# Performance work log

Hardware: AMD Instinct MI355X
Metric: run time of the kernel (lower is better)

The kernel has to match this reference:

```python
import jax, jax.numpy as jnp
import numpy as np

D_MODEL = 1024
NUM_HEADS = 16
D_K = D_MODEL // NUM_HEADS
THETA = 10000.0


def setup_inputs() -> dict:
    key = jax.random.key(0)
    ks = jax.random.split(key, 5)
    b, s = 4, 1024
    std = 1.0 / np.sqrt(D_MODEL)
    x = jax.random.normal(ks[0], (b, s, D_MODEL), dtype=jnp.float32)
    token_positions = jnp.tile(jnp.arange(s, dtype=jnp.int64)[None, :], (b, 1))
    Wq = jax.random.truncated_normal(ks[1], -3.0, 3.0, (D_MODEL, D_MODEL), jnp.float32) * std
    Wk = jax.random.truncated_normal(ks[2], -3.0, 3.0, (D_MODEL, D_MODEL), jnp.float32) * std
    Wv = jax.random.truncated_normal(ks[3], -3.0, 3.0, (D_MODEL, D_MODEL), jnp.float32) * std
    Wo = jax.random.truncated_normal(ks[4], -3.0, 3.0, (D_MODEL, D_MODEL), jnp.float32) * std
    return {"x": x, "token_positions": token_positions,
            "Wq": Wq, "Wk": Wk, "Wv": Wv, "Wo": Wo}


def _apply_rope(x):
    # x: [b, h, s, d_k]; source uses row index i (ignores token_positions)
    s, d = x.shape[-2], x.shape[-1]
    pos = jnp.arange(s, dtype=jnp.float32)                      # [s]
    kidx = jnp.arange(0, d, 2, dtype=jnp.float32)               # [d/2]
    ang = pos[:, None] / (THETA ** (kidx / d))                  # [s, d/2]
    cos, sin = jnp.cos(ang), jnp.sin(ang)
    x_even, x_odd = x[..., 0::2], x[..., 1::2]                  # [b,h,s,d/2]
    out_even = x_even * cos - x_odd * sin
    out_odd = x_even * sin + x_odd * cos
    return jnp.stack([out_even, out_odd], axis=-1).reshape(x.shape)


def reference(x, token_positions, Wq, Wk, Wv, Wo):
    b, s, _ = x.shape
    # Linear: einsum '... din, dout din -> ... dout'  => x @ W.T
    q = jnp.einsum('bsd,ed->bse', x, Wq)
    k = jnp.einsum('bsd,ed->bse', x, Wk)
    v = jnp.einsum('bsd,ed->bse', x, Wv)
    # split heads -> [b, h, s, d_k]
    def split(t):
        return t.reshape(b, s, NUM_HEADS, D_K).transpose(0, 2, 1, 3)
    q, k, v = split(q), split(k), split(v)
    q = _apply_rope(q)
    k = _apply_rope(k)
    scores = jnp.einsum('bhqd,bhkd->bhqk', q, k) / np.sqrt(D_K)
    causal = jnp.tril(jnp.ones((s, s), dtype=bool))
    scores = jnp.where(causal, scores, -jnp.inf)
    attn = jax.nn.softmax(scores, axis=-1)
    out = jnp.einsum('bhqk,bhkd->bhqd', attn, v)
    out = out.transpose(0, 2, 1, 3).reshape(b, s, D_MODEL)
    return jnp.einsum('bsd,ed->bse', out, Wo)
```

## Files before the change

kernel.cpp:

```cpp
#include <hip/hip_runtime.h>

typedef __attribute__((ext_vector_type(8))) short short8;
typedef __attribute__((ext_vector_type(8))) __bf16 bf16x8;
typedef __attribute__((ext_vector_type(4))) float f32x4;
typedef __attribute__((ext_vector_type(4))) float float4v;
typedef __attribute__((ext_vector_type(4))) unsigned short ushort4v;
typedef __attribute__((ext_vector_type(2))) unsigned uint2v;

#define AS1 __attribute__((address_space(1)))
#define AS3 __attribute__((address_space(3)))

#define BATCH 4
#define SEQ 1024
#define DM 1024
#define NH 16
#define DKH 64
#define MROWS (BATCH * SEQ)
#define N3 (3 * DM)

static __device__ __forceinline__ unsigned short f2bf(float f) {
  unsigned u = __builtin_bit_cast(unsigned, f);
  u += 0x7FFFu + ((u >> 16) & 1u);
  return (unsigned short)(u >> 16);
}
static __device__ __forceinline__ float bf2f(unsigned short h) {
  return __builtin_bit_cast(float, ((unsigned)h) << 16);
}
static __device__ __forceinline__ unsigned cvt_pk_bf16(float lo, float hi) {
  unsigned r;
  asm("v_cvt_pk_bf16_f32 %0, %1, %2" : "=v"(r) : "v"(lo), "v"(hi));
  return r;
}
static __device__ __forceinline__ f32x4 mfma16(short8 a, short8 b, f32x4 c) {
  return __builtin_amdgcn_mfma_f32_16x16x32_bf16(
      __builtin_bit_cast(bf16x8, a), __builtin_bit_cast(bf16x8, b), c, 0, 0, 0);
}

__global__ __launch_bounds__(256) void convert_kernel(
    const float* __restrict__ x, const float* __restrict__ wq,
    const float* __restrict__ wk, const float* __restrict__ wv,
    const float* __restrict__ wo, unsigned short* __restrict__ xb,
    unsigned short* __restrict__ wqkv, unsigned short* __restrict__ wob) {
  size_t i4 = ((size_t)blockIdx.x * 256 + threadIdx.x) * 4;
  const size_t SZX = (size_t)MROWS * DM;
  const size_t SZW = (size_t)DM * DM;
  const float* src;
  unsigned short* dst;
  size_t off;
  if (i4 < SZX) {
    src = x; dst = xb; off = i4;
  } else if (i4 < SZX + SZW) {
    src = wq; dst = wqkv; off = i4 - SZX;
  } else if (i4 < SZX + 2 * SZW) {
    src = wk; dst = wqkv + SZW; off = i4 - SZX - SZW;
  } else if (i4 < SZX + 3 * SZW) {
    src = wv; dst = wqkv + 2 * SZW; off = i4 - SZX - 2 * SZW;
  } else {
    src = wo; dst = wob; off = i4 - SZX - 3 * SZW;
  }
  float4v v = *(const float4v*)(src + off);
  uint2v o;
  o.x = cvt_pk_bf16(v.x, v.y);
  o.y = cvt_pk_bf16(v.z, v.w);
  *(uint2v*)(dst + off) = o;
}

static __device__ __forceinline__ void store_c(float* p, float v) { *p = v; }
static __device__ __forceinline__ void store_c(unsigned short* p, float v) { *p = f2bf(v); }

template <typename OutT>
__global__ __launch_bounds__(256) void gemm_bt(
    const unsigned short* __restrict__ A, const unsigned short* __restrict__ B,
    OutT* __restrict__ C, int M, int N, int K) {
  __shared__ char sA[16384];
  __shared__ char sB[16384];
  const int tid = threadIdx.x, w = tid >> 6, lane = tid & 63;
  const int g = lane >> 4, r = lane & 15;
  const int m0 = blockIdx.y * 128, n0 = blockIdx.x * 128;
  const int wm = (w >> 1) * 64, wn = (w & 1) * 64;
  f32x4 acc[4][4] = {};
  for (int k0 = 0; k0 < K; k0 += 64) {
#pragma unroll
    for (int c = 0; c < 4; ++c) {
      int p = c * 4096 + tid * 16;
      int o = p ^ (((p >> 7) & 7) << 4);
      int row = o >> 7, colb = o & 127;
      const char* ga = (const char*)(A + (size_t)(m0 + row) * K + k0) + colb;
      const char* gb = (const char*)(B + (size_t)(n0 + row) * K + k0) + colb;
      __builtin_amdgcn_global_load_lds((const AS1 void*)ga,
                                       (AS3 void*)(sA + c * 4096 + (w << 10)), 16, 0, 0);
      __builtin_amdgcn_global_load_lds((const AS1 void*)gb,
                                       (AS3 void*)(sB + c * 4096 + (w << 10)), 16, 0, 0);
    }
    __syncthreads();
#pragma unroll
    for (int kk = 0; kk < 2; ++kk) {
      short8 af[4], bfr[4];
#pragma unroll
      for (int i = 0; i < 4; ++i) {
        int ra = wm + i * 16 + r;
        af[i] = *(const short8*)(sA + (((ra << 7) + (kk << 6) + (g << 4)) ^ ((ra & 7) << 4)));
        int rb = wn + i * 16 + r;
        bfr[i] = *(const short8*)(sB + (((rb << 7) + (kk << 6) + (g << 4)) ^ ((rb & 7) << 4)));
      }
#pragma unroll
      for (int i = 0; i < 4; ++i)
#pragma unroll
        for (int j = 0; j < 4; ++j) acc[i][j] = mfma16(af[i], bfr[j], acc[i][j]);
    }
    __syncthreads();
  }
#pragma unroll
  for (int i = 0; i < 4; ++i)
#pragma unroll
    for (int j = 0; j < 4; ++j)
#pragma unroll
      for (int jj = 0; jj < 4; ++jj) {
        int row = m0 + wm + i * 16 + g * 4 + jj;
        int col = n0 + wn + j * 16 + r;
        store_c(&C[(size_t)row * N + col], acc[i][j][jj]);
      }
}

__global__ __launch_bounds__(256) void rope_tv(const unsigned short* __restrict__ cf,
                                               unsigned short* __restrict__ qb,
                                               unsigned short* __restrict__ kb,
                                               unsigned short* __restrict__ vt) {
  __shared__ unsigned short tile[64][72];
  const int bid = blockIdx.x;
  if (bid < 8192) {
    int i = bid * 256 + threadIdx.x;
    int k = i & 31, h = (i >> 5) & 15, s = (i >> 9) & 1023, b = i >> 19;
    float freq = __expf(-(float)k * 0.28782313662425572f);
    float ang = (float)s * freq;
    float sn, cs;
    __sincosf(ang, &sn, &cs);
    const unsigned short* src = cf + (size_t)(b * SEQ + s) * N3 + h * DKH + 2 * k;
    float qe = bf2f(src[0]), qo = bf2f(src[1]);
    float ke = bf2f(src[DM]), ko = bf2f(src[DM + 1]);
    float q0 = (qe * cs - qo * sn) * 0.125f;
    float q1 = (qe * sn + qo * cs) * 0.125f;
    float k0 = ke * cs - ko * sn;
    float k1 = ke * sn + ko * cs;
    size_t dsto = (size_t)((b * NH + h) * SEQ + s) * DKH + 2 * k;
    *(unsigned*)(qb + dsto) = cvt_pk_bf16(q0, q1);
    *(unsigned*)(kb + dsto) = cvt_pk_bf16(k0, k1);
  } else {
    int t = bid - 8192;
    int bh = t >> 4, b = bh >> 4, h = bh & 15, s0 = (t & 15) * 64;
    int tt = threadIdx.x, row = tt >> 2, c0 = (tt & 3) * 16;
    const unsigned short* src = cf + (size_t)(b * SEQ + s0 + row) * N3 + 2 * DM + h * DKH + c0;
    short8 v0 = *(const short8*)src;
    short8 v1 = *(const short8*)(src + 8);
    *(short8*)&tile[row][c0] = v0;
    *(short8*)&tile[row][c0 + 8] = v1;
    __syncthreads();
    unsigned short* dst = vt + ((size_t)bh * DKH + row) * SEQ + s0 + c0;
    short8 o0, o1;
#pragma unroll
    for (int j = 0; j < 8; ++j) o0[j] = (short)tile[c0 + j][row];
#pragma unroll
    for (int j = 0; j < 8; ++j) o1[j] = (short)tile[c0 + 8 + j][row];
    *(short8*)dst = o0;
    *(short8*)(dst + 8) = o1;
  }
}

__global__ __launch_bounds__(256) void attn_kernel(const unsigned short* __restrict__ qb,
                                                   const unsigned short* __restrict__ kb,
                                                   const unsigned short* __restrict__ vt,
                                                   unsigned short* __restrict__ ob) {
  __shared__ char kl[2][8192];
  __shared__ char vl[2][8192];
  __shared__ unsigned short plds[4][2][1024];
  const int bx = blockIdx.x, bh = blockIdx.y, b = bh >> 4, h = bh & 15;
  const int qlo = bx, qhi = 15 - bx;
  const int tid = threadIdx.x, w = tid >> 6, lane = tid & 63;
  const int g = lane >> 4, r = lane & 15;
  const unsigned short* Q = qb + (size_t)bh * SEQ * DKH;
  const char* Kp = (const char*)(kb + (size_t)bh * SEQ * DKH);
  const char* Vp = (const char*)(vt + (size_t)bh * DKH * SEQ);

  const int p0 = (w << 10) + lane * 16;
  const int p1 = p0 + 4096;
  const int o0 = p0 ^ (((p0 >> 7) & 7) << 4);
  const int o1 = p1 ^ (((p1 >> 7) & 7) << 4);
  const int r0 = o0 >> 7, c0 = o0 & 127, r1 = o1 >> 7, c1 = o1 & 127;
  const size_t ks0 = (size_t)r0 * 128 + c0, ks1 = (size_t)r1 * 128 + c1;
  const size_t vs0 = (size_t)r0 * 2048 + c0, vs1 = (size_t)r1 * 2048 + c1;

#define STAGE_KV(bi, kt)                                                          \
  do {                                                                            \
    const char* kbase = Kp + (size_t)(kt) * 8192;                                 \
    const char* vbase = Vp + (size_t)(kt) * 128;                                  \
    __builtin_amdgcn_global_load_lds((const AS1 void*)(kbase + ks0),              \
                                     (AS3 void*)(kl[bi] + p0), 16, 0, 0);         \
    __builtin_amdgcn_global_load_lds((const AS1 void*)(kbase + ks1),              \
                                     (AS3 void*)(kl[bi] + p1), 16, 0, 0);         \
    __builtin_amdgcn_global_load_lds((const AS1 void*)(vbase + vs0),              \
                                     (AS3 void*)(vl[bi] + p0), 16, 0, 0);         \
    __builtin_amdgcn_global_load_lds((const AS1 void*)(vbase + vs1),              \
                                     (AS3 void*)(vl[bi] + p1), 16, 0, 0);         \
  } while (0)

  short8 qfL0, qfL1, qfH0, qfH1;
  {
    int qrL = qlo * 64 + w * 16 + r;
    int qrH = qhi * 64 + w * 16 + r;
    qfL0 = *(const short8*)(Q + (size_t)qrL * DKH + g * 8);
    qfL1 = *(const short8*)(Q + (size_t)qrL * DKH + 32 + g * 8);
    qfH0 = *(const short8*)(Q + (size_t)qrH * DKH + g * 8);
    qfH1 = *(const short8*)(Q + (size_t)qrH * DKH + 32 + g * 8);
  }
  f32x4 oaccL[4] = {}, oaccH[4] = {};
  float mrunL = -1e30f, lrunL = 0.f, mrunH = -1e30f, lrunH = 0.f;
  const int qgH = qhi * 64 + w * 16 + r;
  const int qgL = qlo * 64 + w * 16 + r;
  char* pbH = (char*)&plds[w][0][0];
  char* pbL = (char*)&plds[w][1][0];

  STAGE_KV(0, 0);
  __syncthreads();

  for (int kt = 0; kt <= qhi; ++kt) {
    if (kt < qhi) STAGE_KV((kt + 1) & 1, kt + 1);
    const bool doLo = (kt <= qlo);
    const char* kb_ = kl[kt & 1];
    const char* vb_ = vl[kt & 1];
    f32x4 sh[4] = {}, sl[4] = {};
#pragma unroll
    for (int nb = 0; nb < 4; ++nb) {
      int ra = nb * 16 + r;
      short8 kf0 = *(const short8*)(kb_ + ((ra * 128 + g * 16) ^ ((ra & 7) << 4)));
      short8 kf1 = *(const short8*)(kb_ + ((ra * 128 + 64 + g * 16) ^ ((ra & 7) << 4)));
      sh[nb] = mfma16(kf0, qfH0, sh[nb]);
      sh[nb] = mfma16(kf1, qfH1, sh[nb]);
      if (doLo) {
        sl[nb] = mfma16(kf0, qfL0, sl[nb]);
        sl[nb] = mfma16(kf1, qfL1, sl[nb]);
      }
    }
    if (kt == qhi) {
#pragma unroll
      for (int nb = 0; nb < 4; ++nb)
#pragma unroll
        for (int j = 0; j < 4; ++j)
          if (kt * 64 + nb * 16 + g * 4 + j > qgH) sh[nb][j] = -1e30f;
    }
    if (kt == qlo) {
#pragma unroll
      for (int nb = 0; nb < 4; ++nb)
#pragma unroll
        for (int j = 0; j < 4; ++j)
          if (kt * 64 + nb * 16 + g * 4 + j > qgL) sl[nb][j] = -1e30f;
    }
    float sclH, sclL = 1.f;
    {
      float a0 = fmaxf(fmaxf(sh[0][0], sh[0][1]), fmaxf(sh[0][2], sh[0][3]));
      float a1 = fmaxf(fmaxf(sh[1][0], sh[1][1]), fmaxf(sh[1][2], sh[1][3]));
      float a2 = fmaxf(fmaxf(sh[2][0], sh[2][1]), fmaxf(sh[2][2], sh[2][3]));
      float a3 = fmaxf(fmaxf(sh[3][0], sh[3][1]), fmaxf(sh[3][2], sh[3][3]));
      float tm = fmaxf(fmaxf(a0, a1), fmaxf(a2, a3));
      tm = fmaxf(tm, __shfl_xor(tm, 16, 64));
      tm = fmaxf(tm, __shfl_xor(tm, 32, 64));
      float mnew = fmaxf(mrunH, tm);
      sclH = __expf(mrunH - mnew);
      mrunH = mnew;
      float ps = 0.f;
#pragma unroll
      for (int nb = 0; nb < 4; ++nb)
#pragma unroll
        for (int j = 0; j < 4; ++j) {
          float p = __expf(sh[nb][j] - mnew);
          sh[nb][j] = p;
          ps += p;
        }
      ps += __shfl_xor(ps, 16, 64);
      ps += __shfl_xor(ps, 32, 64);
      lrunH = lrunH * sclH + ps;
#pragma unroll
      for (int nb = 0; nb < 4; ++nb) {
        uint2v pk;
        pk.x = cvt_pk_bf16(sh[nb][0], sh[nb][1]);
        pk.y = cvt_pk_bf16(sh[nb][2], sh[nb][3]);
        *(uint2v*)(pbH + ((r * 128 + nb * 32 + g * 8) ^ ((r & 7) << 4))) = pk;
      }
    }
    if (doLo) {
      float a0 = fmaxf(fmaxf(sl[0][0], sl[0][1]), fmaxf(sl[0][2], sl[0][3]));
      float a1 = fmaxf(fmaxf(sl[1][0], sl[1][1]), fmaxf(sl[1][2], sl[1][3]));
      float a2 = fmaxf(fmaxf(sl[2][0], sl[2][1]), fmaxf(sl[2][2], sl[2][3]));
      float a3 = fmaxf(fmaxf(sl[3][0], sl[3][1]), fmaxf(sl[3][2], sl[3][3]));
      float tm = fmaxf(fmaxf(a0, a1), fmaxf(a2, a3));
      tm = fmaxf(tm, __shfl_xor(tm, 16, 64));
      tm = fmaxf(tm, __shfl_xor(tm, 32, 64));
      float mnew = fmaxf(mrunL, tm);
      sclL = __expf(mrunL - mnew);
      mrunL = mnew;
      float ps = 0.f;
#pragma unroll
      for (int nb = 0; nb < 4; ++nb)
#pragma unroll
        for (int j = 0; j < 4; ++j) {
          float p = __expf(sl[nb][j] - mnew);
          sl[nb][j] = p;
          ps += p;
        }
      ps += __shfl_xor(ps, 16, 64);
      ps += __shfl_xor(ps, 32, 64);
      lrunL = lrunL * sclL + ps;
#pragma unroll
      for (int nb = 0; nb < 4; ++nb) {
        uint2v pk;
        pk.x = cvt_pk_bf16(sl[nb][0], sl[nb][1]);
        pk.y = cvt_pk_bf16(sl[nb][2], sl[nb][3]);
        *(uint2v*)(pbL + ((r * 128 + nb * 32 + g * 8) ^ ((r & 7) << 4))) = pk;
      }
    }
#pragma unroll
    for (int db = 0; db < 4; ++db) {
      f32x4 t = oaccH[db];
      t[0] *= sclH; t[1] *= sclH; t[2] *= sclH; t[3] *= sclH;
      oaccH[db] = t;
      if (doLo) {
        f32x4 u = oaccL[db];
        u[0] *= sclL; u[1] *= sclL; u[2] *= sclL; u[3] *= sclL;
        oaccL[db] = u;
      }
    }
    asm volatile("s_waitcnt lgkmcnt(0)" ::: "memory");
    __builtin_amdgcn_sched_barrier(0);
    short8 pfH0 = *(const short8*)(pbH + ((r * 128 + g * 16) ^ ((r & 7) << 4)));
    short8 pfH1 = *(const short8*)(pbH + ((r * 128 + 64 + g * 16) ^ ((r & 7) << 4)));
    short8 pfL0, pfL1;
    if (doLo) {
      pfL0 = *(const short8*)(pbL + ((r * 128 + g * 16) ^ ((r & 7) << 4)));
      pfL1 = *(const short8*)(pbL + ((r * 128 + 64 + g * 16) ^ ((r & 7) << 4)));
    }
#pragma unroll
    for (int db = 0; db < 4; ++db) {
      int rv = db * 16 + r;
      short8 vf0 = *(const short8*)(vb_ + ((rv * 128 + g * 16) ^ ((rv & 7) << 4)));
      short8 vf1 = *(const short8*)(vb_ + ((rv * 128 + 64 + g * 16) ^ ((rv & 7) << 4)));
      oaccH[db] = mfma16(vf0, pfH0, oaccH[db]);
      oaccH[db] = mfma16(vf1, pfH1, oaccH[db]);
      if (doLo) {
        oaccL[db] = mfma16(vf0, pfL0, oaccL[db]);
        oaccL[db] = mfma16(vf1, pfL1, oaccL[db]);
      }
    }
    __syncthreads();
  }
  {
    float invH = 1.f / lrunH;
    unsigned short* orH = ob + (size_t)(b * SEQ + qgH) * DM + h * DKH;
#pragma unroll
    for (int db = 0; db < 4; ++db) {
      uint2v pk;
      pk.x = cvt_pk_bf16(oaccH[db][0] * invH, oaccH[db][1] * invH);
      pk.y = cvt_pk_bf16(oaccH[db][2] * invH, oaccH[db][3] * invH);
      *(uint2v*)(orH + db * 16 + g * 4) = pk;
    }
    float invL = 1.f / lrunL;
    unsigned short* orL = ob + (size_t)(b * SEQ + qgL) * DM + h * DKH;
#pragma unroll
    for (int db = 0; db < 4; ++db) {
      uint2v pk;
      pk.x = cvt_pk_bf16(oaccL[db][0] * invL, oaccL[db][1] * invL);
      pk.y = cvt_pk_bf16(oaccL[db][2] * invL, oaccL[db][3] * invL);
      *(uint2v*)(orL + db * 16 + g * 4) = pk;
    }
  }
#undef STAGE_KV
}

extern "C" void kernel_launch(void* const* d_in, const int* in_sizes, int n_in,
                              void* d_out, int out_size, void* d_ws, size_t ws_size,
                              hipStream_t stream) {
  const float* x = (const float*)d_in[0];
  const float* wq = (const float*)d_in[2];
  const float* wk = (const float*)d_in[3];
  const float* wv = (const float*)d_in[4];
  const float* wo = (const float*)d_in[5];
  char* ws = (char*)d_ws;
  unsigned short* xb = (unsigned short*)(ws);
  unsigned short* wqkv = (unsigned short*)(ws + (8u << 20));
  unsigned short* wob = (unsigned short*)(ws + (14u << 20));
  unsigned short* cf = (unsigned short*)(ws + (16u << 20));
  unsigned short* qbuf = (unsigned short*)(ws + (40u << 20));
  unsigned short* kbuf = (unsigned short*)(ws + (48u << 20));
  unsigned short* vtb = (unsigned short*)(ws + (56u << 20));
  unsigned short* obuf = (unsigned short*)(ws + (64u << 20));
  float* out = (float*)d_out;

  convert_kernel<<<8192, 256, 0, stream>>>(x, wq, wk, wv, wo, xb, wqkv, wob);
  gemm_bt<unsigned short><<<dim3(24, 32), 256, 0, stream>>>(xb, wqkv, cf, MROWS, N3, DM);
  rope_tv<<<9216, 256, 0, stream>>>(cf, qbuf, kbuf, vtb);
  attn_kernel<<<dim3(8, 64), 256, 0, stream>>>(qbuf, kbuf, vtb, obuf);
  gemm_bt<float><<<dim3(8, 32), 256, 0, stream>>>(obuf, wob, out, MROWS, DM, DM);
}
```

Baseline: 113.1 us.

## Vectorize RoPE, add lazy softmax rescaling, and use 128x64 tiles for output GEMM

After: 105.4 us. -6.8%, faster.

```diff
diff --git a/kernel.cpp b/kernel.cpp
--- a/kernel.cpp
+++ b/kernel.cpp
@@ -6,6 +6,7 @@
 typedef __attribute__((ext_vector_type(4))) float float4v;
 typedef __attribute__((ext_vector_type(4))) unsigned short ushort4v;
 typedef __attribute__((ext_vector_type(2))) unsigned uint2v;
+typedef __attribute__((ext_vector_type(4))) unsigned uint4v;
 
 #define AS1 __attribute__((address_space(1)))
 #define AS3 __attribute__((address_space(3)))
@@ -122,31 +123,93 @@
       }
 }
 
+__global__ __launch_bounds__(256) void gemm_n64(
+    const unsigned short* __restrict__ A, const unsigned short* __restrict__ B,
+    float* __restrict__ C, int M, int N, int K) {
+  __shared__ char sA[16384];
+  __shared__ char sB[8192];
+  const int tid = threadIdx.x, w = tid >> 6, lane = tid & 63;
+  const int g = lane >> 4, r = lane & 15;
+  const int m0 = blockIdx.y * 128, n0 = blockIdx.x * 64;
+  const int wm = (w >> 1) * 64, wn = (w & 1) * 32;
+  f32x4 acc[4][2] = {};
+  for (int k0 = 0; k0 < K; k0 += 64) {
+#pragma unroll
+    for (int c = 0; c < 4; ++c) {
+      int p = c * 4096 + tid * 16;
+      int o = p ^ (((p >> 7) & 7) << 4);
+      int row = o >> 7, colb = o & 127;
+      const char* ga = (const char*)(A + (size_t)(m0 + row) * K + k0) + colb;
+      __builtin_amdgcn_global_load_lds((const AS1 void*)ga,
+                                       (AS3 void*)(sA + c * 4096 + (w << 10)), 16, 0, 0);
+      if (c < 2) {
+        const char* gb = (const char*)(B + (size_t)(n0 + row) * K + k0) + colb;
+        __builtin_amdgcn_global_load_lds((const AS1 void*)gb,
+                                         (AS3 void*)(sB + c * 4096 + (w << 10)), 16, 0, 0);
+      }
+    }
+    __syncthreads();
+#pragma unroll
+    for (int kk = 0; kk < 2; ++kk) {
+      short8 af[4], bfr[2];
+#pragma unroll
+      for (int i = 0; i < 4; ++i) {
+        int ra = wm + i * 16 + r;
+        af[i] = *(const short8*)(sA + (((ra << 7) + (kk << 6) + (g << 4)) ^ ((ra & 7) << 4)));
+      }
+#pragma unroll
+      for (int j = 0; j < 2; ++j) {
+        int rb = wn + j * 16 + r;
+        bfr[j] = *(const short8*)(sB + (((rb << 7) + (kk << 6) + (g << 4)) ^ ((rb & 7) << 4)));
+      }
+#pragma unroll
+      for (int i = 0; i < 4; ++i)
+#pragma unroll
+        for (int j = 0; j < 2; ++j) acc[i][j] = mfma16(af[i], bfr[j], acc[i][j]);
+    }
+    __syncthreads();
+  }
+#pragma unroll
+  for (int i = 0; i < 4; ++i)
+#pragma unroll
+    for (int j = 0; j < 2; ++j)
+#pragma unroll
+      for (int jj = 0; jj < 4; ++jj) {
+        int row = m0 + wm + i * 16 + g * 4 + jj;
+        int col = n0 + wn + j * 16 + r;
+        C[(size_t)row * N + col] = acc[i][j][jj];
+      }
+}
+
 __global__ __launch_bounds__(256) void rope_tv(const unsigned short* __restrict__ cf,
                                                unsigned short* __restrict__ qb,
                                                unsigned short* __restrict__ kb,
                                                unsigned short* __restrict__ vt) {
   __shared__ unsigned short tile[64][72];
   const int bid = blockIdx.x;
-  if (bid < 8192) {
+  if (bid < 2048) {
     int i = bid * 256 + threadIdx.x;
-    int k = i & 31, h = (i >> 5) & 15, s = (i >> 9) & 1023, b = i >> 19;
-    float freq = __expf(-(float)k * 0.28782313662425572f);
-    float ang = (float)s * freq;
-    float sn, cs;
-    __sincosf(ang, &sn, &cs);
-    const unsigned short* src = cf + (size_t)(b * SEQ + s) * N3 + h * DKH + 2 * k;
-    float qe = bf2f(src[0]), qo = bf2f(src[1]);
-    float ke = bf2f(src[DM]), ko = bf2f(src[DM + 1]);
-    float q0 = (qe * cs - qo * sn) * 0.125f;
-    float q1 = (qe * sn + qo * cs) * 0.125f;
-    float k0 = ke * cs - ko * sn;
-    float k1 = ke * sn + ko * cs;
-    size_t dsto = (size_t)((b * NH + h) * SEQ + s) * DKH + 2 * k;
-    *(unsigned*)(qb + dsto) = cvt_pk_bf16(q0, q1);
-    *(unsigned*)(kb + dsto) = cvt_pk_bf16(k0, k1);
+    int t8 = i & 7, h = (i >> 3) & 15, s = (i >> 7) & 1023, b = i >> 17;
+    const unsigned short* src = cf + (size_t)(b * SEQ + s) * N3 + h * DKH + t8 * 8;
+    short8 q8 = *(const short8*)src;
+    short8 k8 = *(const short8*)(src + DM);
+    uint4v qo, ko;
+#pragma unroll
+    for (int p = 0; p < 4; ++p) {
+      int kidx = t8 * 4 + p;
+      float freq = __expf(-(float)kidx * 0.28782313662425572f);
+      float sn, cs;
+      __sincosf((float)s * freq, &sn, &cs);
+      float qe = bf2f((unsigned short)q8[2 * p]), qv = bf2f((unsigned short)q8[2 * p + 1]);
+      float ke = bf2f((unsigned short)k8[2 * p]), kv = bf2f((unsigned short)k8[2 * p + 1]);
+      qo[p] = cvt_pk_bf16((qe * cs - qv * sn) * 0.125f, (qe * sn + qv * cs) * 0.125f);
+      ko[p] = cvt_pk_bf16(ke * cs - kv * sn, ke * sn + kv * cs);
+    }
+    size_t dsto = (size_t)((b * NH + h) * SEQ + s) * DKH + t8 * 8;
+    *(uint4v*)(qb + dsto) = qo;
+    *(uint4v*)(kb + dsto) = ko;
   } else {
-    int t = bid - 8192;
+    int t = bid - 2048;
     int bh = t >> 4, b = bh >> 4, h = bh & 15, s0 = (t & 15) * 64;
     int tt = threadIdx.x, row = tt >> 2, c0 = (tt & 3) * 16;
     const unsigned short* src = cf + (size_t)(b * SEQ + s0 + row) * N3 + 2 * DM + h * DKH + c0;
@@ -254,7 +317,6 @@
         for (int j = 0; j < 4; ++j)
           if (kt * 64 + nb * 16 + g * 4 + j > qgL) sl[nb][j] = -1e30f;
     }
-    float sclH, sclL = 1.f;
     {
       float a0 = fmaxf(fmaxf(sh[0][0], sh[0][1]), fmaxf(sh[0][2], sh[0][3]));
       float a1 = fmaxf(fmaxf(sh[1][0], sh[1][1]), fmaxf(sh[1][2], sh[1][3]));
@@ -263,21 +325,30 @@
       float tm = fmaxf(fmaxf(a0, a1), fmaxf(a2, a3));
       tm = fmaxf(tm, __shfl_xor(tm, 16, 64));
       tm = fmaxf(tm, __shfl_xor(tm, 32, 64));
-      float mnew = fmaxf(mrunH, tm);
-      sclH = __expf(mrunH - mnew);
-      mrunH = mnew;
+      if (!__all(tm <= mrunH + 8.f)) {
+        float mnew = fmaxf(mrunH, tm);
+        float scl = __expf(mrunH - mnew);
+        mrunH = mnew;
+        lrunH *= scl;
+#pragma unroll
+        for (int db = 0; db < 4; ++db) {
+          f32x4 t = oaccH[db];
+          t[0] *= scl; t[1] *= scl; t[2] *= scl; t[3] *= scl;
+          oaccH[db] = t;
+        }
+      }
       float ps = 0.f;
 #pragma unroll
       for (int nb = 0; nb < 4; ++nb)
 #pragma unroll
         for (int j = 0; j < 4; ++j) {
-          float p = __expf(sh[nb][j] - mnew);
+          float p = __expf(sh[nb][j] - mrunH);
           sh[nb][j] = p;
           ps += p;
         }
       ps += __shfl_xor(ps, 16, 64);
       ps += __shfl_xor(ps, 32, 64);
-      lrunH = lrunH * sclH + ps;
+      lrunH += ps;
 #pragma unroll
       for (int nb = 0; nb < 4; ++nb) {
         uint2v pk;
@@ -294,38 +365,36 @@
       float tm = fmaxf(fmaxf(a0, a1), fmaxf(a2, a3));
       tm = fmaxf(tm, __shfl_xor(tm, 16, 64));
       tm = fmaxf(tm, __shfl_xor(tm, 32, 64));
-      float mnew = fmaxf(mrunL, tm);
-      sclL = __expf(mrunL - mnew);
-      mrunL = mnew;
+      if (!__all(tm <= mrunL + 8.f)) {
+        float mnew = fmaxf(mrunL, tm);
+        float scl = __expf(mrunL - mnew);
+        mrunL = mnew;
+        lrunL *= scl;
+#pragma unroll
+        for (int db = 0; db < 4; ++db) {
+          f32x4 t = oaccL[db];
+          t[0] *= scl; t[1] *= scl; t[2] *= scl; t[3] *= scl;
+          oaccL[db] = t;
+        }
+      }
       float ps = 0.f;
 #pragma unroll
       for (int nb = 0; nb < 4; ++nb)
 #pragma unroll
         for (int j = 0; j < 4; ++j) {
-          float p = __expf(sl[nb][j] - mnew);
+          float p = __expf(sl[nb][j] - mrunL);
           sl[nb][j] = p;
           ps += p;
         }
       ps += __shfl_xor(ps, 16, 64);
       ps += __shfl_xor(ps, 32, 64);
-      lrunL = lrunL * sclL + ps;
+      lrunL += ps;
 #pragma unroll
       for (int nb = 0; nb < 4; ++nb) {
         uint2v pk;
         pk.x = cvt_pk_bf16(sl[nb][0], sl[nb][1]);
         pk.y = cvt_pk_bf16(sl[nb][2], sl[nb][3]);
         *(uint2v*)(pbL + ((r * 128 + nb * 32 + g * 8) ^ ((r & 7) << 4))) = pk;
-      }
-    }
-#pragma unroll
-    for (int db = 0; db < 4; ++db) {
-      f32x4 t = oaccH[db];
-      t[0] *= sclH; t[1] *= sclH; t[2] *= sclH; t[3] *= sclH;
-      oaccH[db] = t;
-      if (doLo) {
-        f32x4 u = oaccL[db];
-        u[0] *= sclL; u[1] *= sclL; u[2] *= sclL; u[3] *= sclL;
-        oaccL[db] = u;
       }
     }
     asm volatile("s_waitcnt lgkmcnt(0)" ::: "memory");
@@ -395,7 +464,7 @@
 
   convert_kernel<<<8192, 256, 0, stream>>>(x, wq, wk, wv, wo, xb, wqkv, wob);
   gemm_bt<unsigned short><<<dim3(24, 32), 256, 0, stream>>>(xb, wqkv, cf, MROWS, N3, DM);
-  rope_tv<<<9216, 256, 0, stream>>>(cf, qbuf, kbuf, vtb);
+  rope_tv<<<3072, 256, 0, stream>>>(cf, qbuf, kbuf, vtb);
   attn_kernel<<<dim3(8, 64), 256, 0, stream>>>(qbuf, kbuf, vtb, obuf);
-  gemm_bt<float><<<dim3(8, 32), 256, 0, stream>>>(obuf, wob, out, MROWS, DM, DM);
-}
+  gemm_n64<<<dim3(16, 32), 256, 0, stream>>>(obuf, wob, out, MROWS, DM, DM);
+}
```
